# Optimization experiments

Measured on AMD Instinct MI355X. Metric: run time of the kernel, lower is better.

Reference implementation:

```python
import jax, jax.numpy as jnp
import numpy as np

INF = 1000000000000.0
HEAD_SIZE = 64
HEADS = 12
MAX_LENGTH = 512


def _rope_tables(dim, max_length):
    inv_freq = 1.0 / (10000.0 ** (jnp.arange(0, dim, 2, dtype=jnp.float32) / dim))
    t = jnp.arange(max_length, dtype=jnp.float32)
    freqs = t[:, None] * inv_freq[None, :]  # [L, dim/2]
    return jnp.sin(freqs), jnp.cos(freqs)


def _apply_rope(t, sin, cos):
    # t: [B, L, d]; sin/cos: [L, d/2]
    t1, t2 = t[..., 0::2], t[..., 1::2]
    out = jnp.stack([t1 * cos - t2 * sin, t1 * sin + t2 * cos], axis=-1)
    return out.reshape(t.shape)


def setup_inputs() -> dict:
    key = jax.random.key(0)
    k1, k2, k3, k4, k5 = jax.random.split(key, 5)
    B, L, H = 16, 512, 1024
    inputs = jax.random.normal(k1, (B, L, H), dtype=jnp.float32)
    attention_mask = jnp.ones((B, L), dtype=jnp.float32)
    s1 = 1.0 / np.sqrt(H)
    s2 = 1.0 / np.sqrt(HEAD_SIZE * 2)
    W1 = jax.random.normal(k2, (H, HEAD_SIZE * 2), dtype=jnp.float32) * s1
    b1 = jax.random.normal(k3, (HEAD_SIZE * 2,), dtype=jnp.float32) * s1
    W2 = jax.random.normal(k4, (HEAD_SIZE * 2, HEADS * 2), dtype=jnp.float32) * s2
    b2 = jax.random.normal(k5, (HEADS * 2,), dtype=jnp.float32) * s2
    return {"inputs": inputs, "attention_mask": attention_mask,
            "W1": W1, "b1": b1, "W2": W2, "b2": b2}


def reference(inputs, attention_mask, W1, b1, W2, b2):
    B, L, _ = inputs.shape
    x = inputs @ W1 + b1                      # [B, L, 2*head_size]
    qw, kw = x[..., 0::2], x[..., 1::2]        # [B, L, head_size] each
    sin, cos = _rope_tables(HEAD_SIZE, MAX_LENGTH)
    sin, cos = sin[:L], cos[:L]
    qw = _apply_rope(qw, sin, cos)
    kw = _apply_rope(kw, sin, cos)
    logits = jnp.einsum('bmd,bnd->bmn', qw, kw) / (HEAD_SIZE ** 0.5)  # [B, L, L]
    bias = jnp.swapaxes(x @ W2 + b2, 1, 2) / 2.0                       # [B, 2*heads, L]
    # logits[b,h,m,n] = score[b,m,n] + bias_even[b,h,n] + bias_odd[b,h,m]
    logits = logits[:, None] + bias[:, 0::2, None, :] + bias[:, 1::2, :, None]
    attn_mask = 1.0 - attention_mask[:, None, None, :] * attention_mask[:, None, :, None]
    logits = logits - attn_mask * INF
    tril = jnp.tril(jnp.ones((L, L), dtype=logits.dtype), k=-1)
    logits = logits - tril * INF
    return logits
```

## Files before the change

### kernel.cpp

```cpp
#include <hip/hip_runtime.h>
#include <hip/hip_bf16.h>

typedef short bf16x8 __attribute__((ext_vector_type(8)));
typedef float f32x4 __attribute__((ext_vector_type(4)));
typedef unsigned short u16;
typedef unsigned short u16x8 __attribute__((ext_vector_type(8)));

#define FINF 1.0e12f

__device__ __forceinline__ u16 f2b(float f) {
  union { float f; unsigned int u; } x; x.f = f;
  unsigned int r = x.u + 0x7fffu + ((x.u >> 16) & 1u);
  return (u16)(r >> 16);
}

__global__ __launch_bounds__(256) void k0_w1frag(const float* __restrict__ W1,
                                                 u16* __restrict__ w1f) {
  int idx = blockIdx.x * 256 + threadIdx.x;
  int k = idx >> 7, c = idx & 127;
  float v = W1[idx];
  int chunk = k >> 6, kk = k & 63;
  int ks = kk >> 5, km = kk & 31, kg = km >> 3, i = km & 7;
  int nt = c >> 4, ln = c & 15;
  int dst = chunk * 8192 + (nt * 2 + ks) * 512 + (kg * 16 + ln) * 8 + i;
  w1f[dst] = f2b(v);
}

__global__ __launch_bounds__(256) void k1_prep(
    const float* __restrict__ inputs, const u16* __restrict__ w1f,
    const float* __restrict__ b1, const float* __restrict__ W2,
    const float* __restrict__ b2,
    u16* __restrict__ qw, u16* __restrict__ kw,
    float* __restrict__ biasE, float* __restrict__ biasO) {
  __shared__ u16 Al[32 * 64];
  __shared__ u16 Wl[8192];
  __shared__ float xt[32 * 132];
  __shared__ float w2t[24 * 132];

  int t = threadIdx.x;
  int lane = t & 63, w = t >> 6;
  int r0 = blockIdx.x * 32;
  int b = r0 >> 9, l0 = r0 & 511;

  #pragma unroll
  for (int i = 0; i < 12; ++i) {
    int idx = t + i * 256;
    int k = idx / 24, c = idx - k * 24;
    w2t[c * 132 + k] = W2[idx];
  }

  f32x4 acc[4];
  #pragma unroll
  for (int nti = 0; nti < 4; ++nti) acc[nti] = (f32x4){0.f, 0.f, 0.f, 0.f};

  int wr = (w & 1) * 16;
  int wnt = (w >> 1) * 4;

  const float4* wsrcAll = (const float4*)w1f;
  for (int ch = 0; ch < 16; ++ch) {
    {
      int row = t >> 3, ks8 = (t & 7) * 8;
      const float4* src =
          (const float4*)&inputs[(size_t)(r0 + row) * 1024 + ch * 64 + ks8];
      float4 f0 = src[0], f1 = src[1];
      u16x8 uv;
      uv[0] = f2b(f0.x); uv[1] = f2b(f0.y); uv[2] = f2b(f0.z); uv[3] = f2b(f0.w);
      uv[4] = f2b(f1.x); uv[5] = f2b(f1.y); uv[6] = f2b(f1.z); uv[7] = f2b(f1.w);
      int byt = (row * 128 + (t & 7) * 16) ^ ((row & 7) << 4);
      *(u16x8*)((char*)Al + byt) = uv;
    }
    {
      const float4* wsrc = wsrcAll + ch * 1024;
      float4* wdst = (float4*)Wl;
      #pragma unroll
      for (int i = 0; i < 4; ++i) wdst[t + i * 256] = wsrc[t + i * 256];
    }
    __syncthreads();
    int arow = wr + (lane & 15);
    int hi = lane >> 4;
    #pragma unroll
    for (int ks = 0; ks < 2; ++ks) {
      int cb = ks * 64 + hi * 16;
      bf16x8 a = *(const bf16x8*)((const char*)Al +
                                  ((arow * 128 + cb) ^ ((arow & 7) << 4)));
      #pragma unroll
      for (int nti = 0; nti < 4; ++nti) {
        int nt = wnt + nti;
        bf16x8 bb = *(const bf16x8*)&Wl[((nt * 2 + ks) * 64 + lane) * 8];
        acc[nti] = __builtin_amdgcn_mfma_f32_16x16x32_bf16(a, bb, acc[nti], 0, 0, 0);
      }
    }
    __syncthreads();
  }

  #pragma unroll
  for (int nti = 0; nti < 4; ++nti) {
    int c = (wnt + nti) * 16 + (lane & 15);
    float b1v = b1[c];
    #pragma unroll
    for (int r = 0; r < 4; ++r) {
      int row = wr + ((lane >> 4) << 2) + r;
      xt[row * 132 + c] = acc[nti][r] + b1v;
    }
  }
  __syncthreads();

  {
    int r = t >> 3, jb = (t & 7) * 4;
    int l = l0 + r;
    float fl = (float)l;
    u16x8 qv, kv;
    #pragma unroll
    for (int p = 0; p < 4; ++p) {
      int j = jb + p;
      float4 x4 = *(const float4*)&xt[r * 132 + 4 * j];
      float invf = exp2f(-0.4152410118609203f * (float)j);
      float ang = fl * invf;
      float rev = ang * 0.15915494309189535f;
      rev = rev - floorf(rev);
      float sv, cv;
      __sincosf(rev * 6.2831853071795864f, &sv, &cv);
      qv[2 * p] = f2b(x4.x * cv - x4.z * sv);
      qv[2 * p + 1] = f2b(x4.x * sv + x4.z * cv);
      kv[2 * p] = f2b(x4.y * cv - x4.w * sv);
      kv[2 * p + 1] = f2b(x4.y * sv + x4.w * cv);
    }
    size_t base = ((size_t)(b * 512 + l)) * 64 + jb * 2;
    *(u16x8*)&qw[base] = qv;
    *(u16x8*)&kw[base] = kv;
  }

  if (t < 192) {
    int c = t >> 3;
    int rg = (t & 7) * 4;
    float s0 = b2[c], s1 = s0, s2 = s0, s3 = s0;
    #pragma unroll
    for (int k4 = 0; k4 < 32; ++k4) {
      float4 wv = *(const float4*)&w2t[c * 132 + k4 * 4];
      float4 x0 = *(const float4*)&xt[(rg + 0) * 132 + k4 * 4];
      float4 x1 = *(const float4*)&xt[(rg + 1) * 132 + k4 * 4];
      float4 x2 = *(const float4*)&xt[(rg + 2) * 132 + k4 * 4];
      float4 x3 = *(const float4*)&xt[(rg + 3) * 132 + k4 * 4];
      s0 += x0.x * wv.x + x0.y * wv.y + x0.z * wv.z + x0.w * wv.w;
      s1 += x1.x * wv.x + x1.y * wv.y + x1.z * wv.z + x1.w * wv.w;
      s2 += x2.x * wv.x + x2.y * wv.y + x2.z * wv.z + x2.w * wv.w;
      s3 += x3.x * wv.x + x3.y * wv.y + x3.z * wv.z + x3.w * wv.w;
    }
    int h = c >> 1;
    size_t o = ((size_t)(b * 12 + h)) * 512 + l0 + rg;
    float4 sv = {s0 * 0.5f, s1 * 0.5f, s2 * 0.5f, s3 * 0.5f};
    if (c & 1) *(float4*)&biasO[o] = sv;
    else       *(float4*)&biasE[o] = sv;
  }
}

__global__ __launch_bounds__(256) void k2_main(
    const u16* __restrict__ qw, const u16* __restrict__ kw,
    const float* __restrict__ biasE, const float* __restrict__ biasO,
    const float* __restrict__ amask, float* __restrict__ out) {
  __shared__ char smem[24448];
  u16* Q = (u16*)smem;
  u16* K = (u16*)(smem + 8192);
  float* qkL = (float*)smem;
  float* BN = (float*)(smem + 17408);
  float* BM = (float*)(smem + 17408 + 3264);
  float* AMm = (float*)(smem + 17408 + 6528);
  float* AMn = AMm + 64;

  int t = threadIdx.x;
  int lane = t & 63, w = t >> 6;
  int n0 = blockIdx.x * 64, m0 = blockIdx.y * 64, b = blockIdx.z;
  bool skip = (m0 >= n0 + 64);

  if (!skip) {
    int row = t >> 2, sg = t & 3;
    const u16x8* qsrc = (const u16x8*)&qw[((size_t)(b * 512 + m0 + row)) * 64 + sg * 16];
    u16x8 q0 = qsrc[0], q1 = qsrc[1];
    const u16x8* ksrc = (const u16x8*)&kw[((size_t)(b * 512 + n0 + row)) * 64 + sg * 16];
    u16x8 k0v = ksrc[0], k1v = ksrc[1];
    int swz = (row & 7) << 4;
    int byt = row * 128 + sg * 32;
    *(u16x8*)((char*)Q + ((byt) ^ swz)) = q0;
    *(u16x8*)((char*)Q + ((byt + 16) ^ swz)) = q1;
    *(u16x8*)((char*)K + ((byt) ^ swz)) = k0v;
    *(u16x8*)((char*)K + ((byt + 16) ^ swz)) = k1v;
  }
  if (t < 192) {
    int h = t >> 4, kq = t & 15;
    *(float4*)&BN[h * 68 + kq * 4] =
        *(const float4*)&biasE[((size_t)(b * 12 + h)) * 512 + n0 + kq * 4];
    *(float4*)&BM[h * 68 + kq * 4] =
        *(const float4*)&biasO[((size_t)(b * 12 + h)) * 512 + m0 + kq * 4];
  } else if (t < 224) {
    int i = t - 192;
    if (i < 16) *(float4*)&AMm[i * 4] = *(const float4*)&amask[b * 512 + m0 + i * 4];
    else { int ii = i - 16; *(float4*)&AMn[ii * 4] = *(const float4*)&amask[b * 512 + n0 + ii * 4]; }
  }
  __syncthreads();

  if (!skip) {
    f32x4 acc[4];
    #pragma unroll
    for (int nt = 0; nt < 4; ++nt) acc[nt] = (f32x4){0.f, 0.f, 0.f, 0.f};
    int mrow = w * 16 + (lane & 15);
    int hi = lane >> 4;
    #pragma unroll
    for (int ks = 0; ks < 2; ++ks) {
      int cb = ks * 64 + hi * 16;
      bf16x8 a = *(const bf16x8*)((const char*)Q +
                                  ((mrow * 128 + cb) ^ ((mrow & 7) << 4)));
      #pragma unroll
      for (int nt = 0; nt < 4; ++nt) {
        int nr = nt * 16 + (lane & 15);
        bf16x8 bb = *(const bf16x8*)((const char*)K +
                                     ((nr * 128 + cb) ^ ((nr & 7) << 4)));
        acc[nt] = __builtin_amdgcn_mfma_f32_16x16x32_bf16(a, bb, acc[nt], 0, 0, 0);
      }
    }
    __syncthreads();
    #pragma unroll
    for (int nt = 0; nt < 4; ++nt)
      #pragma unroll
      for (int r = 0; r < 4; ++r)
        qkL[(w * 16 + hi * 4 + r) * 68 + nt * 16 + (lane & 15)] = acc[nt][r];
    __syncthreads();
  }

  int a15 = t & 15, mb = t >> 4;
  float amn0 = AMn[a15 * 4 + 0], amn1 = AMn[a15 * 4 + 1];
  float amn2 = AMn[a15 * 4 + 2], amn3 = AMn[a15 * 4 + 3];
  float vals[4][4];
  #pragma unroll
  for (int mi = 0; mi < 4; ++mi) {
    int m = mb + 16 * mi;
    int mg = m0 + m;
    float amm = AMm[m];
    int ng = n0 + a15 * 4;
    float p0 = (1.f - amm * amn0) * FINF + ((mg > ng + 0) ? FINF : 0.f);
    float p1 = (1.f - amm * amn1) * FINF + ((mg > ng + 1) ? FINF : 0.f);
    float p2 = (1.f - amm * amn2) * FINF + ((mg > ng + 2) ? FINF : 0.f);
    float p3 = (1.f - amm * amn3) * FINF + ((mg > ng + 3) ? FINF : 0.f);
    if (!skip) {
      float4 qk = *(const float4*)&qkL[m * 68 + a15 * 4];
      vals[mi][0] = qk.x * 0.125f - p0;
      vals[mi][1] = qk.y * 0.125f - p1;
      vals[mi][2] = qk.z * 0.125f - p2;
      vals[mi][3] = qk.w * 0.125f - p3;
    } else {
      vals[mi][0] = -p0; vals[mi][1] = -p1; vals[mi][2] = -p2; vals[mi][3] = -p3;
    }
  }

  size_t outbase = (size_t)(b * 12) * 262144 + (size_t)m0 * 512 + n0 + a15 * 4;
  #pragma unroll
  for (int h = 0; h < 12; ++h) {
    float4 bn = *(const float4*)&BN[h * 68 + a15 * 4];
    #pragma unroll
    for (int mi = 0; mi < 4; ++mi) {
      int m = mb + 16 * mi;
      float bm = BM[h * 68 + m];
      float4 v;
      v.x = vals[mi][0] + bn.x + bm;
      v.y = vals[mi][1] + bn.y + bm;
      v.z = vals[mi][2] + bn.z + bm;
      v.w = vals[mi][3] + bn.w + bm;
      *(float4*)&out[outbase + (size_t)h * 262144 + (size_t)m * 512] = v;
    }
  }
}

extern "C" void kernel_launch(void* const* d_in, const int* in_sizes, int n_in,
                              void* d_out, int out_size, void* d_ws, size_t ws_size,
                              hipStream_t stream) {
  const float* inputs = (const float*)d_in[0];
  const float* amask  = (const float*)d_in[1];
  const float* W1     = (const float*)d_in[2];
  const float* b1     = (const float*)d_in[3];
  const float* W2     = (const float*)d_in[4];
  const float* b2     = (const float*)d_in[5];
  float* out = (float*)d_out;

  char* ws = (char*)d_ws;
  u16* qw      = (u16*)(ws);
  u16* kw      = (u16*)(ws + (1u << 20));
  float* biasE = (float*)(ws + (2u << 20));
  float* biasO = (float*)(ws + (2u << 20) + 393216u);
  u16* w1f     = (u16*)(ws + (2u << 20) + 786432u);

  k0_w1frag<<<512, 256, 0, stream>>>(W1, w1f);
  k1_prep<<<256, 256, 0, stream>>>(inputs, w1f, b1, W2, b2, qw, kw, biasE, biasO);
  k2_main<<<dim3(8, 8, 16), 256, 0, stream>>>(qw, kw, biasE, biasO, amask, out);
}
```

Baseline: 59.64 us.

## Double-buffer projection GEMM staging and use nontemporal stores for logits output

The prep kernel's K-loop now prefetches the next chunk of inputs and W1 fragments into registers while MFMAs run on the current shared-memory buffer, writing into a second buffer so only one barrier per iteration is needed. Shared memory is merged into a single aliased buffer, with the later xt tile reusing the GEMM staging space. The output kernel writes logits with nontemporal stores so the large streamed output does not pollute the cache. The costs are higher register use from prefetch registers and a larger LDS footprint, which may reduce occupancy.

```diff
diff --git a/kernel.cpp b/kernel.cpp
--- a/kernel.cpp
+++ b/kernel.cpp
@@ -32,10 +32,9 @@
     const float* __restrict__ b2,
     u16* __restrict__ qw, u16* __restrict__ kw,
     float* __restrict__ biasE, float* __restrict__ biasO) {
-  __shared__ u16 Al[32 * 64];
-  __shared__ u16 Wl[8192];
-  __shared__ float xt[32 * 132];
-  __shared__ float w2t[24 * 132];
+  __shared__ __align__(16) char smem[53632];
+  float* w2t = (float*)(smem + 40960);
+  float* xt  = (float*)smem;
 
   int t = threadIdx.x;
   int lane = t & 63, w = t >> 6;
@@ -56,42 +55,63 @@
   int wr = (w & 1) * 16;
   int wnt = (w >> 1) * 4;
 
+  int arow_s = t >> 3;
+  const float* ain = &inputs[(size_t)(r0 + arow_s) * 1024 + (t & 7) * 8];
+  int abyt = (arow_s * 128 + (t & 7) * 16) ^ ((arow_s & 7) << 4);
   const float4* wsrcAll = (const float4*)w1f;
+
+  float4 a0 = *(const float4*)(ain);
+  float4 a1 = *(const float4*)(ain + 4);
+  float4 wr0 = wsrcAll[t];
+  float4 wr1 = wsrcAll[t + 256];
+  float4 wr2 = wsrcAll[t + 512];
+  float4 wr3 = wsrcAll[t + 768];
+  {
+    u16x8 av;
+    av[0] = f2b(a0.x); av[1] = f2b(a0.y); av[2] = f2b(a0.z); av[3] = f2b(a0.w);
+    av[4] = f2b(a1.x); av[5] = f2b(a1.y); av[6] = f2b(a1.z); av[7] = f2b(a1.w);
+    *(u16x8*)(smem + abyt) = av;
+    float4* wd = (float4*)(smem + 8192);
+    wd[t] = wr0; wd[t + 256] = wr1; wd[t + 512] = wr2; wd[t + 768] = wr3;
+  }
+  __syncthreads();
+
   for (int ch = 0; ch < 16; ++ch) {
+    if (ch < 15) {
+      a0 = *(const float4*)(ain + (ch + 1) * 64);
+      a1 = *(const float4*)(ain + (ch + 1) * 64 + 4);
+      const float4* wsrc = wsrcAll + (ch + 1) * 1024;
+      wr0 = wsrc[t]; wr1 = wsrc[t + 256]; wr2 = wsrc[t + 512]; wr3 = wsrc[t + 768];
+    }
     {
-      int row = t >> 3, ks8 = (t & 7) * 8;
-      const float4* src =
-          (const float4*)&inputs[(size_t)(r0 + row) * 1024 + ch * 64 + ks8];
-      float4 f0 = src[0], f1 = src[1];
-      u16x8 uv;
-      uv[0] = f2b(f0.x); uv[1] = f2b(f0.y); uv[2] = f2b(f0.z); uv[3] = f2b(f0.w);
-      uv[4] = f2b(f1.x); uv[5] = f2b(f1.y); uv[6] = f2b(f1.z); uv[7] = f2b(f1.w);
-      int byt = (row * 128 + (t & 7) * 16) ^ ((row & 7) << 4);
-      *(u16x8*)((char*)Al + byt) = uv;
-    }
-    {
-      const float4* wsrc = wsrcAll + ch * 1024;
-      float4* wdst = (float4*)Wl;
+      const char* Ab = smem + (ch & 1) * 4096;
+      const u16* Wb = (const u16*)(smem + 8192 + (ch & 1) * 16384);
+      int arow = wr + (lane & 15);
+      int hi = lane >> 4;
       #pragma unroll
-      for (int i = 0; i < 4; ++i) wdst[t + i * 256] = wsrc[t + i * 256];
+      for (int ks = 0; ks < 2; ++ks) {
+        int cb = ks * 64 + hi * 16;
+        bf16x8 a = *(const bf16x8*)(Ab + ((arow * 128 + cb) ^ ((arow & 7) << 4)));
+        #pragma unroll
+        for (int nti = 0; nti < 4; ++nti) {
+          int nt = wnt + nti;
+          bf16x8 bb = *(const bf16x8*)&Wb[((nt * 2 + ks) * 64 + lane) * 8];
+          acc[nti] = __builtin_amdgcn_mfma_f32_16x16x32_bf16(a, bb, acc[nti], 0, 0, 0);
+        }
+      }
+    }
+    if (ch < 15) {
+      int q = (ch + 1) & 1;
+      u16x8 av;
+      av[0] = f2b(a0.x); av[1] = f2b(a0.y); av[2] = f2b(a0.z); av[3] = f2b(a0.w);
+      av[4] = f2b(a1.x); av[5] = f2b(a1.y); av[6] = f2b(a1.z); av[7] = f2b(a1.w);
+      *(u16x8*)(smem + q * 4096 + abyt) = av;
+      float4* wd = (float4*)(smem + 8192 + q * 16384);
+      wd[t] = wr0; wd[t + 256] = wr1; wd[t + 512] = wr2; wd[t + 768] = wr3;
     }
     __syncthreads();
-    int arow = wr + (lane & 15);
-    int hi = lane >> 4;
-    #pragma unroll
-    for (int ks = 0; ks < 2; ++ks) {
-      int cb = ks * 64 + hi * 16;
-      bf16x8 a = *(const bf16x8*)((const char*)Al +
-                                  ((arow * 128 + cb) ^ ((arow & 7) << 4)));
-      #pragma unroll
-      for (int nti = 0; nti < 4; ++nti) {
-        int nt = wnt + nti;
-        bf16x8 bb = *(const bf16x8*)&Wl[((nt * 2 + ks) * 64 + lane) * 8];
-        acc[nti] = __builtin_amdgcn_mfma_f32_16x16x32_bf16(a, bb, acc[nti], 0, 0, 0);
-      }
-    }
-    __syncthreads();
-  }
+  }
+  __syncthreads();
 
   #pragma unroll
   for (int nti = 0; nti < 4; ++nti) {
@@ -259,12 +279,13 @@
     for (int mi = 0; mi < 4; ++mi) {
       int m = mb + 16 * mi;
       float bm = BM[h * 68 + m];
-      float4 v;
-      v.x = vals[mi][0] + bn.x + bm;
-      v.y = vals[mi][1] + bn.y + bm;
-      v.z = vals[mi][2] + bn.z + bm;
-      v.w = vals[mi][3] + bn.w + bm;
-      *(float4*)&out[outbase + (size_t)h * 262144 + (size_t)m * 512] = v;
+      f32x4 v;
+      v[0] = vals[mi][0] + bn.x + bm;
+      v[1] = vals[mi][1] + bn.y + bm;
+      v[2] = vals[mi][2] + bn.z + bm;
+      v[3] = vals[mi][3] + bn.w + bm;
+      __builtin_nontemporal_store(v,
+          (f32x4*)&out[outbase + (size_t)h * 262144 + (size_t)m * 512]);
     }
   }
 }
```

New measurement: 63.75 us. 6.9% more time.
